# Optimization experiments

Measured on AMD Instinct MI355X. Metric: run time of the kernel, lower is better.

Reference implementation:

```python
import jax, jax.numpy as jnp
import numpy as np

B, S, H = 1, 2048, 2048
NH = 16
HS = H // NH  # 128
NEG = -65504.0  # fp16 min used as additive mask value


def setup_inputs() -> dict:
    key = jax.random.key(0)
    k1, k2, k3, k4, k5 = jax.random.split(key, 5)
    hidden_states = jax.random.normal(k1, (B, S, H), dtype=jnp.float32)
    # causal left-to-right mask: 1 where attention allowed
    ltor_mask = jnp.tril(jnp.ones((S, S), dtype=jnp.float32))[None, None, :, :]
    W_qkv = jax.random.normal(k2, (H, 3 * H), dtype=jnp.float32) * (1.0 / np.sqrt(H))
    b_qkv = jax.random.normal(k3, (3 * H,), dtype=jnp.float32) * 0.01
    W_dense = jax.random.normal(k4, (H, H), dtype=jnp.float32) * (1.0 / np.sqrt(H))
    b_dense = jax.random.normal(k5, (H,), dtype=jnp.float32) * 0.01
    return {"hidden_states": hidden_states, "ltor_mask": ltor_mask,
            "W_qkv": W_qkv, "b_qkv": b_qkv, "W_dense": W_dense, "b_dense": b_dense}


def reference(hidden_states, ltor_mask, W_qkv, b_qkv, W_dense, b_dense):
    b, s, h = hidden_states.shape
    # fused QKV projection, then split along last dim (matches split_tensor_along_last_dim)
    qkv = hidden_states @ W_qkv + b_qkv  # [b, s, 3h]
    q, k, v = jnp.split(qkv, 3, axis=-1)
    q = q.reshape(b, s, NH, HS)
    k = k.reshape(b, s, NH, HS)
    v = v.reshape(b, s, NH, HS)
    scale = 1.0 / np.sqrt(HS)  # softmax_scale=None -> 1/sqrt(headdim)
    scores = jnp.einsum('bqhd,bkhd->bhqk', q, k) * scale
    scores = scores + NEG * (1.0 - ltor_mask)  # additive mask, [b,1,s,s] broadcast over heads
    probs = jax.nn.softmax(scores, axis=-1)
    ctx = jnp.einsum('bhqk,bkhd->bqhd', probs, v).reshape(b, s, h)
    out = ctx @ W_dense + b_dense  # output_dropout is identity in eval
    return out
```

## Files before the change

kernel.cpp:

```cpp
#include <hip/hip_runtime.h>
#include <math.h>

#define S_LEN 2048
#define HDIM  2048
#define NHEAD 16
#define HSZ   128
#define H3    6144

typedef __attribute__((ext_vector_type(8))) short bf16x8;
typedef __attribute__((ext_vector_type(4))) float f32x4;

__device__ inline ushort f2bf(float f) {
    union { float f; unsigned u; } c; c.f = f;
    unsigned u = c.u;
    return (ushort)((u + 0x7fffu + ((u >> 16) & 1u)) >> 16);
}
__device__ inline ushort f2bf_trunc(float f) {
    union { float f; unsigned u; } c; c.f = f;
    return (ushort)(c.u >> 16);
}

__global__ __launch_bounds__(256) void prep(
    const float* __restrict__ X,    ushort* __restrict__ Xb,
    const float* __restrict__ Wqkv, ushort* __restrict__ Wqt,
    const float* __restrict__ Wd,   ushort* __restrict__ Wdt)
{
    __shared__ ushort t[64][66];
    const int bid = blockIdx.x;
    const int tid = threadIdx.x;

    if (bid < 4096) {
        int i = bid * 1024 + tid * 4;
        float4 v = *(const float4*)(X + i);
        ushort4 o;
        o.x = f2bf(v.x); o.y = f2bf(v.y); o.z = f2bf(v.z); o.w = f2bf(v.w);
        *(ushort4*)(Xb + i) = o;
        return;
    }

    const float* W; ushort* Wt; int K, N, n0, k0;
    if (bid < 7168) {
        const int b = bid - 4096;
        W = Wqkv; Wt = Wqt; K = HDIM; N = H3;
        n0 = (b % 96) * 64; k0 = (b / 96) * 64;
    } else {
        const int b = bid - 7168;
        W = Wd; Wt = Wdt; K = HDIM; N = HDIM;
        n0 = (b % 32) * 64; k0 = (b / 32) * 64;
    }
    const int tx = tid & 15;
    const int ty = tid >> 4;
    #pragma unroll
    for (int p = 0; p < 4; p++) {
        const int k = p * 16 + ty;
        float4 v = *(const float4*)(&W[(size_t)(k0 + k) * N + n0 + tx * 4]);
        t[k][tx * 4 + 0] = f2bf(v.x);
        t[k][tx * 4 + 1] = f2bf(v.y);
        t[k][tx * 4 + 2] = f2bf(v.z);
        t[k][tx * 4 + 3] = f2bf(v.w);
    }
    __syncthreads();
    #pragma unroll
    for (int p = 0; p < 4; p++) {
        const int n = p * 16 + ty;
        ushort4 o;
        o.x = t[tx * 4 + 0][n];
        o.y = t[tx * 4 + 1][n];
        o.z = t[tx * 4 + 2][n];
        o.w = t[tx * 4 + 3][n];
        *(ushort4*)(&Wt[(size_t)(n0 + n) * K + k0 + tx * 4]) = o;
    }
}

__global__ __launch_bounds__(256) void transpose_v(const ushort* __restrict__ qkvb,
                                                   ushort* __restrict__ Vtb) {
    __shared__ ushort t[64][66];
    const int s0 = blockIdx.x * 64;
    const int d0 = blockIdx.y * 64;
    const int tx = threadIdx.x & 15;
    const int ty = threadIdx.x >> 4;
    #pragma unroll
    for (int p = 0; p < 4; p++) {
        const int s = p * 16 + ty;
        ushort4 v = *(const ushort4*)(&qkvb[(size_t)(s0 + s) * H3 + 2 * HDIM + d0 + tx * 4]);
        *(ushort4*)(&t[s][tx * 4]) = v;
    }
    __syncthreads();
    #pragma unroll
    for (int p = 0; p < 4; p++) {
        const int d = p * 16 + ty;
        ushort4 o;
        o.x = t[tx * 4 + 0][d];
        o.y = t[tx * 4 + 1][d];
        o.z = t[tx * 4 + 2][d];
        o.w = t[tx * 4 + 3][d];
        *(ushort4*)(&Vtb[(size_t)(d0 + d) * S_LEN + s0 + tx * 4]) = o;
    }
}

__global__ __launch_bounds__(512, 2) void gemm_qkv_v2(
    const ushort* __restrict__ A, const ushort* __restrict__ Bt,
    const float* __restrict__ bias, ushort* __restrict__ Cb,
    int M, int N, int K)
{
    __shared__ __align__(16) ushort lds[2][256 * 64 + 192 * 64];

    const int tid  = threadIdx.x;
    const int m0   = blockIdx.y * 256;
    const int n0   = blockIdx.x * 192;
    const int w    = tid >> 6;
    const int wm   = w >> 1;
    const int wn   = w & 1;
    const int lane = tid & 63;
    const int quad = lane >> 4;
    const int l16  = lane & 15;

    const int rdsw = l16 & 7;

    f32x4 acc[4][6] = {};

    const int T = K / 64;

    auto stageA = [&](int kt, int b) {
        const int k0 = kt * 64;
        #pragma unroll
        for (int r = 0; r < 4; r++) {
            const int c    = r * 512 + tid;
            const int row  = c >> 3;
            const int csw  = ((c & 7) ^ (row & 7)) * 8;
            const ushort* ga = A + (size_t)(m0 + row) * K + k0 + csw;
            __builtin_amdgcn_global_load_lds(
                (const __attribute__((address_space(1))) void*)ga,
                (__attribute__((address_space(3))) void*)(&lds[b][0] + c * 8), 16, 0, 0);
        }
    };
    auto stageB = [&](int kt, int b) {
        const int k0 = kt * 64;
        #pragma unroll
        for (int r = 0; r < 3; r++) {
            const int c    = r * 512 + tid;
            const int row  = c >> 3;
            const int csw  = ((c & 7) ^ (row & 7)) * 8;
            const ushort* gb = Bt + (size_t)(n0 + row) * K + k0 + csw;
            __builtin_amdgcn_global_load_lds(
                (const __attribute__((address_space(1))) void*)gb,
                (__attribute__((address_space(3))) void*)(&lds[b][16384] + c * 8), 16, 0, 0);
        }
    };

    stageA(0, 0);
    stageB(0, 0);

    for (int t = 0; t < T; t++) {
        const int b = t & 1;
        if (t + 1 < T) {
            stageA(t + 1, b ^ 1);
            asm volatile("s_waitcnt vmcnt(4)" ::: "memory");
        } else {
            asm volatile("s_waitcnt vmcnt(0)" ::: "memory");
        }
        asm volatile("s_barrier" ::: "memory");

        const ushort* bA = &lds[b][0];
        const ushort* bB = &lds[b][16384];

        bf16x8 af[4][2], bqa[3][2], bqb[3][2];

        #pragma unroll
        for (int i = 0; i < 4; i++)
            #pragma unroll
            for (int kc = 0; kc < 2; kc++)
                af[i][kc] = *(const bf16x8*)(bA + (wm * 64 + i * 16 + l16) * 64
                                               + ((((kc << 2) | quad) ^ rdsw) * 8));
        #pragma unroll
        for (int j = 0; j < 3; j++)
            #pragma unroll
            for (int kc = 0; kc < 2; kc++)
                bqa[j][kc] = *(const bf16x8*)(bB + (wn * 96 + j * 16 + l16) * 64
                                                + ((((kc << 2) | quad) ^ rdsw) * 8));
        asm volatile("s_barrier" ::: "memory");
        __builtin_amdgcn_s_setprio(1);
        #pragma unroll
        for (int i = 0; i < 4; i++)
            #pragma unroll
            for (int j = 0; j < 3; j++)
                #pragma unroll
                for (int kc = 0; kc < 2; kc++)
                    acc[i][j] = __builtin_amdgcn_mfma_f32_16x16x32_bf16(
                        af[i][kc], bqa[j][kc], acc[i][j], 0, 0, 0);
        __builtin_amdgcn_s_setprio(0);
        asm volatile("s_barrier" ::: "memory");

        if (t + 1 < T) stageB(t + 1, b ^ 1);

        #pragma unroll
        for (int j = 0; j < 3; j++)
            #pragma unroll
            for (int kc = 0; kc < 2; kc++)
                bqb[j][kc] = *(const bf16x8*)(bB + (wn * 96 + (3 + j) * 16 + l16) * 64
                                                + ((((kc << 2) | quad) ^ rdsw) * 8));
        asm volatile("s_barrier" ::: "memory");
        __builtin_amdgcn_s_setprio(1);
        #pragma unroll
        for (int i = 0; i < 4; i++)
            #pragma unroll
            for (int j = 0; j < 3; j++)
                #pragma unroll
                for (int kc = 0; kc < 2; kc++)
                    acc[i][3 + j] = __builtin_amdgcn_mfma_f32_16x16x32_bf16(
                        af[i][kc], bqb[j][kc], acc[i][3 + j], 0, 0, 0);
        __builtin_amdgcn_s_setprio(0);
        asm volatile("s_waitcnt lgkmcnt(0)" ::: "memory");
        asm volatile("s_barrier" ::: "memory");
    }

    #pragma unroll
    for (int i = 0; i < 4; i++) {
        #pragma unroll
        for (int r = 0; r < 4; r++) {
            const int m = m0 + wm * 64 + i * 16 + quad * 4 + r;
            #pragma unroll
            for (int j = 0; j < 6; j++) {
                const int n = n0 + wn * 96 + j * 16 + l16;
                float v  = acc[i][j][r] + bias[n];
                float vp = __shfl_xor(v, 1, 64);
                unsigned both = (unsigned)f2bf(v) | ((unsigned)f2bf(vp) << 16);
                if ((l16 & 1) == 0)
                    *(unsigned*)(Cb + (size_t)m * N + n) = both;
            }
        }
    }
}

__global__ __launch_bounds__(256) void gemm_dense(
    const ushort* __restrict__ A, const ushort* __restrict__ Bt,
    const float* __restrict__ bias, float* __restrict__ C)
{
    __shared__ ushort sA[2 * 64 * 32];
    __shared__ ushort sB[2 * 128 * 32];

    const int tid  = threadIdx.x;
    const int m0   = blockIdx.y * 64;
    const int n0   = blockIdx.x * 128;
    const int w    = tid >> 6;
    const int lane = tid & 63;
    const int quad = lane >> 4;
    const int l16  = lane & 15;
    const int wr   = (w >> 1) * 32;
    const int wc   = (w & 1) * 64;

    f32x4 acc[2][4] = {};

    for (int k0 = 0; k0 < HDIM; k0 += 64) {
        #pragma unroll
        for (int iss = 0; iss < 2; iss++) {
            const int li  = iss * 256 + tid;
            const int c   = li >> 8;
            const int row = (li >> 2) & 63;
            const int kc  = (li & 3) * 8;
            const ushort* ga = A + (size_t)(m0 + row) * HDIM + k0 + c * 32 + kc;
            __builtin_amdgcn_global_load_lds(
                (const __attribute__((address_space(1))) void*)ga,
                (__attribute__((address_space(3))) void*)(sA + li * 8), 16, 0, 0);
        }
        #pragma unroll
        for (int iss = 0; iss < 4; iss++) {
            const int li  = iss * 256 + tid;
            const int c   = li >> 9;
            const int row = (li >> 2) & 127;
            const int kc  = (li & 3) * 8;
            const ushort* gb = Bt + (size_t)(n0 + row) * HDIM + k0 + c * 32 + kc;
            __builtin_amdgcn_global_load_lds(
                (const __attribute__((address_space(1))) void*)gb,
                (__attribute__((address_space(3))) void*)(sB + li * 8), 16, 0, 0);
        }
        __syncthreads();

        #pragma unroll
        for (int c = 0; c < 2; c++) {
            bf16x8 af[2], bq[4];
            #pragma unroll
            for (int i = 0; i < 2; i++)
                af[i] = *(const bf16x8*)(sA + c * 2048 + (wr + i * 16 + l16) * 32 + quad * 8);
            #pragma unroll
            for (int j = 0; j < 4; j++)
                bq[j] = *(const bf16x8*)(sB + c * 4096 + (wc + j * 16 + l16) * 32 + quad * 8);

            #pragma unroll
            for (int i = 0; i < 2; i++)
                #pragma unroll
                for (int j = 0; j < 4; j++)
                    acc[i][j] = __builtin_amdgcn_mfma_f32_16x16x32_bf16(
                        af[i], bq[j], acc[i][j], 0, 0, 0);
        }
        __syncthreads();
    }

    #pragma unroll
    for (int i = 0; i < 2; i++)
        #pragma unroll
        for (int r = 0; r < 4; r++) {
            const int m = m0 + wr + i * 16 + quad * 4 + r;
            #pragma unroll
            for (int j = 0; j < 4; j++) {
                const int n = n0 + wc + j * 16 + l16;
                C[(size_t)m * HDIM + n] = acc[i][j][r] + bias[n];
            }
        }
}

__global__ __launch_bounds__(256) void attn_mfma(
    const ushort* __restrict__ qkvb, const ushort* __restrict__ Vtb,
    ushort* __restrict__ ctxb)
{
    __shared__ __align__(16) ushort sK [2][64 * 128];
    __shared__ __align__(16) ushort sVt[2][128 * 64];
    __shared__ __align__(16) ushort Ps [4 * 1024];

    const int tid  = threadIdx.x;
    const int bid  = blockIdx.x;
    const int h    = bid & 15;
    const int qt   = (bid < 256) ? (31 - (bid >> 4)) : ((bid - 256) >> 4);
    const int q0   = qt * 64;
    const int w    = tid >> 6;
    const int lane = tid & 63;
    const int quad = lane >> 4;
    const int l16  = lane & 15;
    const int qr0  = q0 + w * 16;

    const float scale = 0.08838834764831845f;

    bf16x8 qf[4];
    #pragma unroll
    for (int c = 0; c < 4; c++)
        qf[c] = *(const bf16x8*)(qkvb + (size_t)(qr0 + l16) * H3 + h * HSZ + c * 32 + quad * 8);

    f32x4 o[8] = {};
    float lsum[4] = {0.f, 0.f, 0.f, 0.f};

    const int nt   = qt + 1;
    const int skey = tid >> 2;
    const int sq8  = tid & 3;

    auto stage = [&](int kt, int b) {
        const int k0 = kt * 64;
        #pragma unroll
        for (int iss = 0; iss < 4; iss++) {
            const int li = iss * 256 + tid;
            const ushort* g = qkvb + (size_t)(k0 + skey) * H3 + HDIM + h * HSZ + iss * 32 + sq8 * 8;
            __builtin_amdgcn_global_load_lds(
                (const __attribute__((address_space(1))) void*)g,
                (__attribute__((address_space(3))) void*)(&sK[b][0] + li * 8), 16, 0, 0);
        }
        #pragma unroll
        for (int iss = 0; iss < 4; iss++) {
            const int li = iss * 256 + tid;
            const int c  = li >> 9;
            const int d  = (li >> 2) & 127;
            const ushort* g = Vtb + (size_t)(h * HSZ + d) * S_LEN + k0 + c * 32 + (li & 3) * 8;
            __builtin_amdgcn_global_load_lds(
                (const __attribute__((address_space(1))) void*)g,
                (__attribute__((address_space(3))) void*)(&sVt[b][0] + li * 8), 16, 0, 0);
        }
    };

    stage(0, 0);
    const int wofs = w * 1024;

    for (int kt = 0; kt < nt; kt++) {
        const int b  = kt & 1;
        const int k0 = kt * 64;

        if (kt + 1 < nt) {
            stage(kt + 1, b ^ 1);
            asm volatile("s_waitcnt vmcnt(8)" ::: "memory");
        } else {
            asm volatile("s_waitcnt vmcnt(0)" ::: "memory");
        }
        asm volatile("s_barrier" ::: "memory");

        const ushort* bK = &sK[b][0];
        const ushort* bV = &sVt[b][0];

        f32x4 sacc[4] = {};
        #pragma unroll
        for (int jt = 0; jt < 4; jt++)
            #pragma unroll
            for (int c = 0; c < 4; c++) {
                bf16x8 kf = *(const bf16x8*)(bK + c * 2048 + (jt * 16 + l16) * 32 + quad * 8);
                sacc[jt] = __builtin_amdgcn_mfma_f32_16x16x32_bf16(qf[c], kf, sacc[jt], 0, 0, 0);
            }

        float p[4][4];
        if (kt == nt - 1) {
            #pragma unroll
            for (int jt = 0; jt < 4; jt++) {
                const int key = k0 + jt * 16 + l16;
                #pragma unroll
                for (int r = 0; r < 4; r++) {
                    float e = __expf(sacc[jt][r] * scale);
                    if (key > qr0 + quad * 4 + r) e = 0.f;
                    p[jt][r] = e;
                    lsum[r] += e;
                }
            }
        } else {
            #pragma unroll
            for (int jt = 0; jt < 4; jt++)
                #pragma unroll
                for (int r = 0; r < 4; r++) {
                    float e = __expf(sacc[jt][r] * scale);
                    p[jt][r] = e;
                    lsum[r] += e;
                }
        }

        #pragma unroll
        for (int jt = 0; jt < 4; jt++) {
            const int cpan = jt >> 1;
            const int lch  = (jt & 1) * 2 + (l16 >> 3);
            const int phys = lch ^ quad;
            #pragma unroll
            for (int r = 0; r < 4; r++) {
                const int row = quad * 4 + r;
                Ps[wofs + cpan * 512 + row * 32 + phys * 8 + (l16 & 7)] = f2bf_trunc(p[jt][r]);
            }
        }

        #pragma unroll
        for (int c = 0; c < 2; c++) {
            const int pph = quad ^ (l16 >> 2);
            bf16x8 pf = *(const bf16x8*)(Ps + wofs + c * 512 + l16 * 32 + pph * 8);
            #pragma unroll
            for (int ht = 0; ht < 8; ht++) {
                bf16x8 vf = *(const bf16x8*)(bV + c * 4096 + (ht * 16 + l16) * 32 + quad * 8);
                o[ht] = __builtin_amdgcn_mfma_f32_16x16x32_bf16(pf, vf, o[ht], 0, 0, 0);
            }
        }

        asm volatile("s_waitcnt lgkmcnt(0)" ::: "memory");
        asm volatile("s_barrier" ::: "memory");
    }

    float invl[4];
    #pragma unroll
    for (int r = 0; r < 4; r++) {
        float ls = lsum[r];
        #pragma unroll
        for (int off = 1; off < 16; off <<= 1)
            ls += __shfl_xor(ls, off, 64);
        invl[r] = 1.0f / ls;
    }
    #pragma unroll
    for (int ht = 0; ht < 8; ht++) {
        #pragma unroll
        for (int r = 0; r < 4; r++) {
            float v  = o[ht][r] * invl[r];
            float vp = __shfl_xor(v, 1, 64);
            unsigned both = (unsigned)f2bf(v) | ((unsigned)f2bf(vp) << 16);
            if ((l16 & 1) == 0)
                *(unsigned*)(ctxb + (size_t)(qr0 + quad * 4 + r) * HDIM + h * HSZ + ht * 16 + l16) = both;
        }
    }
}

extern "C" void kernel_launch(void* const* d_in, const int* in_sizes, int n_in,
                              void* d_out, int out_size, void* d_ws, size_t ws_size,
                              hipStream_t stream) {
    const float* X    = (const float*)d_in[0];
    const float* Wqkv = (const float*)d_in[2];
    const float* bqkv = (const float*)d_in[3];
    const float* Wd   = (const float*)d_in[4];
    const float* bd   = (const float*)d_in[5];
    float* out = (float*)d_out;

    ushort* Xb   = (ushort*)d_ws;
    ushort* Wqt  = Xb   + (size_t)S_LEN * HDIM;
    ushort* Wdt  = Wqt  + (size_t)H3 * HDIM;
    ushort* ctxb = Wdt  + (size_t)HDIM * HDIM;
    ushort* qkvb = ctxb + (size_t)S_LEN * HDIM;
    ushort* Vtb  = qkvb + (size_t)S_LEN * H3;

    dim3 blk(256);

    prep<<<dim3(8192), blk, 0, stream>>>(X, Xb, Wqkv, Wqt, Wd, Wdt);

    gemm_qkv_v2<<<dim3(H3 / 192, S_LEN / 256), dim3(512), 0, stream>>>(
        Xb, Wqt, bqkv, qkvb, S_LEN, H3, HDIM);

    transpose_v<<<dim3(S_LEN / 64, HDIM / 64), blk, 0, stream>>>(qkvb, Vtb);

    attn_mfma<<<dim3(512), blk, 0, stream>>>(qkvb, Vtb, ctxb);

    gemm_dense<<<dim3(HDIM / 128, S_LEN / 64), blk, 0, stream>>>(
        ctxb, Wdt, bd, out);
}
```

Measured before the change: 278.0 us.

## Deepen QKV GEMM prefetch to two stages with four-phase MFMA schedule

The QKV GEMM now prefetches two K-tiles ahead, reusing the same double-buffered LDS slot. It splits each tile's compute into four quadrant MFMA phases, with the next A and B global-to-LDS copies issued between the phases. The goal is to hide global-load latency better and interleave LDS reads with MFMA work. Because only two LDS buffers serve a two-deep prefetch, correctness depends on the barrier and waitcnt ordering, which adds hazard risk and more barriers per tile.

```diff
diff --git a/kernel.cpp b/kernel.cpp
--- a/kernel.cpp
+++ b/kernel.cpp
@@ -98,7 +98,7 @@
     }
 }
 
-__global__ __launch_bounds__(512, 2) void gemm_qkv_v2(
+__global__ __launch_bounds__(512, 2) void gemm_qkv_v3(
     const ushort* __restrict__ A, const ushort* __restrict__ Bt,
     const float* __restrict__ bias, ushort* __restrict__ Cb,
     int M, int N, int K)
@@ -121,7 +121,8 @@
 
     const int T = K / 64;
 
-    auto stageA = [&](int kt, int b) {
+    auto stageA = [&](int kt) {
+        const int b  = kt & 1;
         const int k0 = kt * 64;
         #pragma unroll
         for (int r = 0; r < 4; r++) {
@@ -134,7 +135,8 @@
                 (__attribute__((address_space(3))) void*)(&lds[b][0] + c * 8), 16, 0, 0);
         }
     };
-    auto stageB = [&](int kt, int b) {
+    auto stageB = [&](int kt) {
+        const int b  = kt & 1;
         const int k0 = kt * 64;
         #pragma unroll
         for (int r = 0; r < 3; r++) {
@@ -148,70 +150,101 @@
         }
     };
 
-    stageA(0, 0);
-    stageB(0, 0);
-
-    for (int t = 0; t < T; t++) {
-        const int b = t & 1;
-        if (t + 1 < T) {
-            stageA(t + 1, b ^ 1);
-            asm volatile("s_waitcnt vmcnt(4)" ::: "memory");
+    stageA(0); stageB(0);
+    stageA(1); stageB(1);
+
+    for (int u = 0; u < T; u++) {
+        const int b = u & 1;
+        if (u == T - 1) {
+            asm volatile("s_waitcnt vmcnt(0)" ::: "memory");
         } else {
-            asm volatile("s_waitcnt vmcnt(0)" ::: "memory");
+            asm volatile("s_waitcnt vmcnt(7)" ::: "memory");
         }
         asm volatile("s_barrier" ::: "memory");
 
         const ushort* bA = &lds[b][0];
         const ushort* bB = &lds[b][16384];
 
-        bf16x8 af[4][2], bqa[3][2], bqb[3][2];
-
-        #pragma unroll
-        for (int i = 0; i < 4; i++)
+        bf16x8 af_lo[2][2], af_hi[2][2], bq_lo[3][2], bq_hi[3][2];
+
+        #pragma unroll
+        for (int i = 0; i < 2; i++)
             #pragma unroll
             for (int kc = 0; kc < 2; kc++)
-                af[i][kc] = *(const bf16x8*)(bA + (wm * 64 + i * 16 + l16) * 64
-                                               + ((((kc << 2) | quad) ^ rdsw) * 8));
+                af_lo[i][kc] = *(const bf16x8*)(bA + (wm * 64 + i * 16 + l16) * 64
+                                                  + ((((kc << 2) | quad) ^ rdsw) * 8));
         #pragma unroll
         for (int j = 0; j < 3; j++)
             #pragma unroll
             for (int kc = 0; kc < 2; kc++)
-                bqa[j][kc] = *(const bf16x8*)(bB + (wn * 96 + j * 16 + l16) * 64
-                                                + ((((kc << 2) | quad) ^ rdsw) * 8));
-        asm volatile("s_barrier" ::: "memory");
+                bq_lo[j][kc] = *(const bf16x8*)(bB + (wn * 96 + j * 16 + l16) * 64
+                                                  + ((((kc << 2) | quad) ^ rdsw) * 8));
+        asm volatile("s_barrier" ::: "memory");
+        asm volatile("s_waitcnt lgkmcnt(0)" ::: "memory");
         __builtin_amdgcn_s_setprio(1);
         #pragma unroll
-        for (int i = 0; i < 4; i++)
+        for (int i = 0; i < 2; i++)
             #pragma unroll
             for (int j = 0; j < 3; j++)
                 #pragma unroll
                 for (int kc = 0; kc < 2; kc++)
                     acc[i][j] = __builtin_amdgcn_mfma_f32_16x16x32_bf16(
-                        af[i][kc], bqa[j][kc], acc[i][j], 0, 0, 0);
+                        af_lo[i][kc], bq_lo[j][kc], acc[i][j], 0, 0, 0);
         __builtin_amdgcn_s_setprio(0);
         asm volatile("s_barrier" ::: "memory");
 
-        if (t + 1 < T) stageB(t + 1, b ^ 1);
+        #pragma unroll
+        for (int i = 0; i < 2; i++)
+            #pragma unroll
+            for (int kc = 0; kc < 2; kc++)
+                af_hi[i][kc] = *(const bf16x8*)(bA + (wm * 64 + (2 + i) * 16 + l16) * 64
+                                                  + ((((kc << 2) | quad) ^ rdsw) * 8));
+        asm volatile("s_barrier" ::: "memory");
+        asm volatile("s_waitcnt lgkmcnt(0)" ::: "memory");
+        __builtin_amdgcn_s_setprio(1);
+        #pragma unroll
+        for (int i = 0; i < 2; i++)
+            #pragma unroll
+            for (int j = 0; j < 3; j++)
+                #pragma unroll
+                for (int kc = 0; kc < 2; kc++)
+                    acc[2 + i][j] = __builtin_amdgcn_mfma_f32_16x16x32_bf16(
+                        af_hi[i][kc], bq_lo[j][kc], acc[2 + i][j], 0, 0, 0);
+        __builtin_amdgcn_s_setprio(0);
+        asm volatile("s_barrier" ::: "memory");
 
         #pragma unroll
         for (int j = 0; j < 3; j++)
             #pragma unroll
             for (int kc = 0; kc < 2; kc++)
-                bqb[j][kc] = *(const bf16x8*)(bB + (wn * 96 + (3 + j) * 16 + l16) * 64
-                                                + ((((kc << 2) | quad) ^ rdsw) * 8));
-        asm volatile("s_barrier" ::: "memory");
+                bq_hi[j][kc] = *(const bf16x8*)(bB + (wn * 96 + (3 + j) * 16 + l16) * 64
+                                                  + ((((kc << 2) | quad) ^ rdsw) * 8));
+        if (u + 2 < T) stageA(u + 2);
+        asm volatile("s_barrier" ::: "memory");
+        asm volatile("s_waitcnt lgkmcnt(0)" ::: "memory");
         __builtin_amdgcn_s_setprio(1);
         #pragma unroll
-        for (int i = 0; i < 4; i++)
+        for (int i = 0; i < 2; i++)
+            #pragma unroll
+            for (int j = 0; j < 3; j++)
+                #pragma unroll
+                for (int kc = 0; kc < 2; kc++)
+                    acc[2 + i][3 + j] = __builtin_amdgcn_mfma_f32_16x16x32_bf16(
+                        af_hi[i][kc], bq_hi[j][kc], acc[2 + i][3 + j], 0, 0, 0);
+        __builtin_amdgcn_s_setprio(0);
+        asm volatile("s_barrier" ::: "memory");
+
+        if (u + 2 < T) stageB(u + 2);
+        __builtin_amdgcn_s_setprio(1);
+        #pragma unroll
+        for (int i = 0; i < 2; i++)
             #pragma unroll
             for (int j = 0; j < 3; j++)
                 #pragma unroll
                 for (int kc = 0; kc < 2; kc++)
                     acc[i][3 + j] = __builtin_amdgcn_mfma_f32_16x16x32_bf16(
-                        af[i][kc], bqb[j][kc], acc[i][3 + j], 0, 0, 0);
+                        af_lo[i][kc], bq_hi[j][kc], acc[i][3 + j], 0, 0, 0);
         __builtin_amdgcn_s_setprio(0);
-        asm volatile("s_waitcnt lgkmcnt(0)" ::: "memory");
-        asm volatile("s_barrier" ::: "memory");
     }
 
     #pragma unroll
@@ -485,7 +518,7 @@
 
     prep<<<dim3(8192), blk, 0, stream>>>(X, Xb, Wqkv, Wqt, Wd, Wdt);
 
-    gemm_qkv_v2<<<dim3(H3 / 192, S_LEN / 256), dim3(512), 0, stream>>>(
+    gemm_qkv_v3<<<dim3(H3 / 192, S_LEN / 256), dim3(512), 0, stream>>>(
         Xb, Wqt, bqkv, qkvb, S_LEN, H3, HDIM);
 
     transpose_v<<<dim3(S_LEN / 64, HDIM / 64), blk, 0, stream>>>(qkvb, Vtb);
```

Measured after the change: 272.8 us. No clear change (-1.9%).

## Shrink QKV GEMM tile to 128x192 with 256 threads and simpler pipeline

Applied to the files above, without the earlier changes.

The QKV projection GEMM moves from 512-thread blocks computing 256x192 tiles to 256-thread blocks computing 128x192 tiles, which doubles the grid to 512 blocks for better CU coverage. The split A/B staging with mid-iteration barriers is replaced by a single stage that prefetches both operands for the next k-step, followed by one load-then-MFMA phase per iteration. This drops barriers and should improve occupancy and load balance, at the cost of lower operand reuse per block and more register pressure from holding all six B fragments at once.

```diff
diff --git a/kernel.cpp b/kernel.cpp
--- a/kernel.cpp
+++ b/kernel.cpp
@@ -98,15 +98,15 @@
     }
 }
 
-__global__ __launch_bounds__(512, 2) void gemm_qkv_v2(
+__global__ __launch_bounds__(256, 2) void gemm_qkv_v4(
     const ushort* __restrict__ A, const ushort* __restrict__ Bt,
     const float* __restrict__ bias, ushort* __restrict__ Cb,
     int M, int N, int K)
 {
-    __shared__ __align__(16) ushort lds[2][256 * 64 + 192 * 64];
+    __shared__ __align__(16) ushort lds[2][128 * 64 + 192 * 64];
 
     const int tid  = threadIdx.x;
-    const int m0   = blockIdx.y * 256;
+    const int m0   = blockIdx.y * 128;
     const int n0   = blockIdx.x * 192;
     const int w    = tid >> 6;
     const int wm   = w >> 1;
@@ -121,51 +121,47 @@
 
     const int T = K / 64;
 
-    auto stageA = [&](int kt, int b) {
+    auto stage = [&](int kt) {
+        const int b  = kt & 1;
         const int k0 = kt * 64;
         #pragma unroll
         for (int r = 0; r < 4; r++) {
-            const int c    = r * 512 + tid;
-            const int row  = c >> 3;
-            const int csw  = ((c & 7) ^ (row & 7)) * 8;
+            const int c   = r * 256 + tid;
+            const int row = c >> 3;
+            const int csw = ((c & 7) ^ (row & 7)) * 8;
             const ushort* ga = A + (size_t)(m0 + row) * K + k0 + csw;
             __builtin_amdgcn_global_load_lds(
                 (const __attribute__((address_space(1))) void*)ga,
                 (__attribute__((address_space(3))) void*)(&lds[b][0] + c * 8), 16, 0, 0);
         }
+        #pragma unroll
+        for (int r = 0; r < 6; r++) {
+            const int c   = r * 256 + tid;
+            const int row = c >> 3;
+            const int csw = ((c & 7) ^ (row & 7)) * 8;
+            const ushort* gb = Bt + (size_t)(n0 + row) * K + k0 + csw;
+            __builtin_amdgcn_global_load_lds(
+                (const __attribute__((address_space(1))) void*)gb,
+                (__attribute__((address_space(3))) void*)(&lds[b][8192] + c * 8), 16, 0, 0);
+        }
     };
-    auto stageB = [&](int kt, int b) {
-        const int k0 = kt * 64;
-        #pragma unroll
-        for (int r = 0; r < 3; r++) {
-            const int c    = r * 512 + tid;
-            const int row  = c >> 3;
-            const int csw  = ((c & 7) ^ (row & 7)) * 8;
-            const ushort* gb = Bt + (size_t)(n0 + row) * K + k0 + csw;
-            __builtin_amdgcn_global_load_lds(
-                (const __attribute__((address_space(1))) void*)gb,
-                (__attribute__((address_space(3))) void*)(&lds[b][16384] + c * 8), 16, 0, 0);
-        }
-    };
-
-    stageA(0, 0);
-    stageB(0, 0);
-
-    for (int t = 0; t < T; t++) {
-        const int b = t & 1;
-        if (t + 1 < T) {
-            stageA(t + 1, b ^ 1);
-            asm volatile("s_waitcnt vmcnt(4)" ::: "memory");
+
+    stage(0);
+
+    for (int u = 0; u < T; u++) {
+        const int b = u & 1;
+        if (u + 1 < T) {
+            stage(u + 1);
+            asm volatile("s_waitcnt vmcnt(10)" ::: "memory");
         } else {
             asm volatile("s_waitcnt vmcnt(0)" ::: "memory");
         }
         asm volatile("s_barrier" ::: "memory");
 
         const ushort* bA = &lds[b][0];
-        const ushort* bB = &lds[b][16384];
-
-        bf16x8 af[4][2], bqa[3][2], bqb[3][2];
-
+        const ushort* bB = &lds[b][8192];
+
+        bf16x8 af[4][2], bq[6][2];
         #pragma unroll
         for (int i = 0; i < 4; i++)
             #pragma unroll
@@ -173,43 +169,23 @@
                 af[i][kc] = *(const bf16x8*)(bA + (wm * 64 + i * 16 + l16) * 64
                                                + ((((kc << 2) | quad) ^ rdsw) * 8));
         #pragma unroll
-        for (int j = 0; j < 3; j++)
+        for (int j = 0; j < 6; j++)
             #pragma unroll
             for (int kc = 0; kc < 2; kc++)
-                bqa[j][kc] = *(const bf16x8*)(bB + (wn * 96 + j * 16 + l16) * 64
-                                                + ((((kc << 2) | quad) ^ rdsw) * 8));
-        asm volatile("s_barrier" ::: "memory");
+                bq[j][kc] = *(const bf16x8*)(bB + (wn * 96 + j * 16 + l16) * 64
+                                               + ((((kc << 2) | quad) ^ rdsw) * 8));
+
         __builtin_amdgcn_s_setprio(1);
         #pragma unroll
         for (int i = 0; i < 4; i++)
             #pragma unroll
-            for (int j = 0; j < 3; j++)
+            for (int j = 0; j < 6; j++)
                 #pragma unroll
                 for (int kc = 0; kc < 2; kc++)
                     acc[i][j] = __builtin_amdgcn_mfma_f32_16x16x32_bf16(
-                        af[i][kc], bqa[j][kc], acc[i][j], 0, 0, 0);
+                        af[i][kc], bq[j][kc], acc[i][j], 0, 0, 0);
         __builtin_amdgcn_s_setprio(0);
-        asm volatile("s_barrier" ::: "memory");
-
-        if (t + 1 < T) stageB(t + 1, b ^ 1);
-
-        #pragma unroll
-        for (int j = 0; j < 3; j++)
-            #pragma unroll
-            for (int kc = 0; kc < 2; kc++)
-                bqb[j][kc] = *(const bf16x8*)(bB + (wn * 96 + (3 + j) * 16 + l16) * 64
-                                                + ((((kc << 2) | quad) ^ rdsw) * 8));
-        asm volatile("s_barrier" ::: "memory");
-        __builtin_amdgcn_s_setprio(1);
-        #pragma unroll
-        for (int i = 0; i < 4; i++)
-            #pragma unroll
-            for (int j = 0; j < 3; j++)
-                #pragma unroll
-                for (int kc = 0; kc < 2; kc++)
-                    acc[i][3 + j] = __builtin_amdgcn_mfma_f32_16x16x32_bf16(
-                        af[i][kc], bqb[j][kc], acc[i][3 + j], 0, 0, 0);
-        __builtin_amdgcn_s_setprio(0);
+
         asm volatile("s_waitcnt lgkmcnt(0)" ::: "memory");
         asm volatile("s_barrier" ::: "memory");
     }
@@ -485,7 +461,7 @@
 
     prep<<<dim3(8192), blk, 0, stream>>>(X, Xb, Wqkv, Wqt, Wd, Wdt);
 
-    gemm_qkv_v2<<<dim3(H3 / 192, S_LEN / 256), dim3(512), 0, stream>>>(
+    gemm_qkv_v4<<<dim3(H3 / 192, S_LEN / 128), blk, 0, stream>>>(
         Xb, Wqt, bqkv, qkvb, S_LEN, H3, HDIM);
 
     transpose_v<<<dim3(S_LEN / 64, HDIM / 64), blk, 0, stream>>>(qkvb, Vtb);
```

Result: no change. 275.9 us (-0.8%).
